# Performance work log

Hardware: AMD Instinct MI355X
Metric: run time of the kernel (lower is better)

Reference implementation:

```python
import jax, jax.numpy as jnp
import numpy as np

DIM = 512
NUM_HEADS = 8
HEAD_DIM = DIM // NUM_HEADS
MAX_SEQ_LEN = 4096
B, L = 2, 4096
LN_EPS = 1e-5


def _rope_cache(max_len, head_dim):
    inv_freq = 1.0 / (10000.0 ** (jnp.arange(0, head_dim, 2, dtype=jnp.float32) / head_dim))
    t = jnp.arange(max_len, dtype=jnp.float32)
    freqs = jnp.einsum('i,j->ij', t, inv_freq)          # [max_len, head_dim//2]
    emb = jnp.concatenate([freqs, freqs], axis=-1)       # [max_len, head_dim]
    return jnp.cos(emb)[None, None], jnp.sin(emb)[None, None]  # [1,1,max_len,head_dim]


def setup_inputs() -> dict:
    key = jax.random.key(0)
    ks = jax.random.split(key, 8)
    s_qkv = 1.0 / np.sqrt(DIM)
    x = jax.random.normal(ks[0], (B, L, DIM), dtype=jnp.float32)
    padding_mask = jax.random.bernoulli(ks[1], 0.1, (B, L))  # True = masked key
    Wqkv = jax.random.uniform(ks[2], (DIM, 3 * DIM), jnp.float32, -s_qkv, s_qkv)
    bqkv = jax.random.uniform(ks[3], (3 * DIM,), jnp.float32, -s_qkv, s_qkv)
    Wproj = jax.random.uniform(ks[4], (DIM, DIM), jnp.float32, -s_qkv, s_qkv)
    bproj = jax.random.uniform(ks[5], (DIM,), jnp.float32, -s_qkv, s_qkv)
    gamma = jnp.ones((DIM,), jnp.float32)
    beta = jnp.zeros((DIM,), jnp.float32)
    cos, sin = _rope_cache(MAX_SEQ_LEN, HEAD_DIM)
    return {"x": x, "padding_mask": padding_mask, "Wqkv": Wqkv, "bqkv": bqkv,
            "Wproj": Wproj, "bproj": bproj, "gamma": gamma, "beta": beta,
            "cos": cos, "sin": sin}


def _rotate_half(t):
    t1, t2 = jnp.split(t, 2, axis=-1)
    return jnp.concatenate([-t2, t1], axis=-1)


def reference(x, padding_mask, Wqkv, bqkv, Wproj, bproj, gamma, beta, cos, sin):
    b, l, d = x.shape
    residual = x
    qkv = (x @ Wqkv + bqkv).reshape(b, l, 3, NUM_HEADS, HEAD_DIM)
    qkv = jnp.transpose(qkv, (2, 0, 3, 1, 4))            # [3,B,H,L,hd]
    q, k, v = qkv[0], qkv[1], qkv[2]
    c = cos[:, :, :l, :]
    s = sin[:, :, :l, :]
    q = q * c + _rotate_half(q) * s
    k = k * c + _rotate_half(k) * s
    scores = jnp.einsum('bhqd,bhkd->bhqk', q, k) / jnp.sqrt(jnp.float32(HEAD_DIM))
    scores = jnp.where(padding_mask[:, None, None, :], -jnp.inf, scores)
    attn = jax.nn.softmax(scores, axis=-1)
    out = jnp.einsum('bhqk,bhkd->bhqd', attn, v)
    out = jnp.transpose(out, (0, 2, 1, 3)).reshape(b, l, d)
    y = out @ Wproj + bproj + residual
    mu = jnp.mean(y, axis=-1, keepdims=True)
    var = jnp.mean(jnp.square(y - mu), axis=-1, keepdims=True)
    return (y - mu) * jax.lax.rsqrt(var + LN_EPS) * gamma + beta
```

## Files before the change

### kernel.cpp

```cpp
#include <hip/hip_runtime.h>
#include <hip/hip_bf16.h>

typedef __bf16 bf16;
typedef __attribute__((ext_vector_type(8))) __bf16 bf16x8;
typedef __attribute__((ext_vector_type(2))) __bf16 bf16x2;
typedef __attribute__((ext_vector_type(4))) float f32x4;
typedef __attribute__((ext_vector_type(16))) float f32x16;
typedef __attribute__((ext_vector_type(4))) unsigned int u32x4;

#define DIMV 512
#define NH 8
#define HDIM 64
#define SEQ 4096
#define BB_ 2
#define M_TOT (BB_ * SEQ)
#define NQKV 1536
#define KVBLK 64

static __device__ __forceinline__ f32x4 mfma16(bf16x8 a, bf16x8 b, f32x4 c) {
  return __builtin_amdgcn_mfma_f32_16x16x32_bf16(a, b, c, 0, 0, 0);
}
static __device__ __forceinline__ f32x16 mfma32(bf16x8 a, bf16x8 b, f32x16 c) {
  return __builtin_amdgcn_mfma_f32_32x32x16_bf16(a, b, c, 0, 0, 0);
}
static __device__ __forceinline__ unsigned pk2(float a, float b) {
  bf16x2 t; t[0] = (bf16)a; t[1] = (bf16)b;
  return __builtin_bit_cast(unsigned, t);
}
static __device__ __forceinline__ void swap32(unsigned& a, unsigned& b) {
  asm("v_permlane32_swap_b32 %0, %1" : "+v"(a), "+v"(b));
}
static __device__ __forceinline__ int swz(int row, int byteoff) {
  return byteoff ^ ((row & 7) << 4);
}

__global__ void prep_w(const float* __restrict__ Wqkv, const float* __restrict__ Wproj,
                       const float* __restrict__ x, const int* __restrict__ mask,
                       bf16* __restrict__ WqkvT, bf16* __restrict__ WprojT,
                       bf16* __restrict__ xb, float* __restrict__ BBias) {
  const int t1 = DIMV * NQKV;
  const int t2 = t1 + DIMV * DIMV;
  const int t3 = t2 + M_TOT * DIMV;
  const int t4 = t3 + BB_ * SEQ;
  for (int i = blockIdx.x * blockDim.x + threadIdx.x; i < t4;
       i += gridDim.x * blockDim.x) {
    if (i < t1) {
      int n = i / DIMV, k = i - n * DIMV;
      WqkvT[i] = (bf16)Wqkv[(size_t)k * NQKV + n];
    } else if (i < t2) {
      int o = i - t1;
      int n = o / DIMV, k = o - n * DIMV;
      WprojT[o] = (bf16)Wproj[(size_t)k * DIMV + n];
    } else if (i < t3) {
      int o = i - t2;
      xb[o] = (bf16)x[o];
    } else {
      int o = i - t3;
      BBias[o] = mask[o] ? -1.0e30f : 0.0f;
    }
  }
}

__global__ __launch_bounds__(256) void gemm1_qkv_rope(
    const bf16* __restrict__ xb, const bf16* __restrict__ WT,
    const float* __restrict__ bqkv, const float* __restrict__ cosT,
    const float* __restrict__ sinT, bf16* __restrict__ Q,
    bf16* __restrict__ Kd, bf16* __restrict__ VT) {
  const int tid = threadIdx.x;
  const int wave = tid >> 6, lane = tid & 63;
  const int l16 = lane & 15, lg = lane >> 4;
  const int Mbase = blockIdx.x * 128 + (wave >> 1) * 64;
  const int Nbase = blockIdx.y * 128 + (wave & 1) * 64;
  const int gblk = (blockIdx.y * 128) >> 9;

  f32x4 acc[4][4] = {};
  if (gblk != 2) {
    for (int k0 = 0; k0 < DIMV; k0 += 32) {
      const int kb = k0 + lg * 8;
      bf16x8 af[4], bfr[4];
#pragma unroll
      for (int r = 0; r < 4; ++r) {
        af[r] = *reinterpret_cast<const bf16x8*>(
            xb + (size_t)(Mbase + r * 16 + l16) * DIMV + kb);
        bfr[r] = *reinterpret_cast<const bf16x8*>(
            WT + (size_t)(Nbase + r * 16 + l16) * DIMV + kb);
      }
#pragma unroll
      for (int mr = 0; mr < 4; ++mr)
#pragma unroll
        for (int nr = 0; nr < 4; ++nr)
          acc[mr][nr] = mfma16(af[mr], bfr[nr], acc[mr][nr]);
    }
#pragma unroll
    for (int mr = 0; mr < 4; ++mr) {
#pragma unroll
      for (int nr = 0; nr < 4; ++nr) {
#pragma unroll
        for (int j = 0; j < 4; ++j) {
          const int n = Nbase + nr * 16 + l16;
          const int m = Mbase + mr * 16 + lg * 4 + j;
          const int rem = n & 511, h = rem >> 6, d = rem & 63;
          const int b = m >> 12, l = m & 4095;
          float val = acc[mr][nr][j] + bqkv[n];
          float pairval = acc[mr][nr ^ 2][j] + bqkv[n ^ 32];
          float c = cosT[l * HDIM + d], s = sinT[l * HDIM + d];
          float o = (d < 32) ? (val * c - pairval * s) : (val * c + pairval * s);
          bf16* dst = (gblk == 0) ? Q : Kd;
          dst[((size_t)(b * NH + h) * SEQ + l) * HDIM + d] = (bf16)o;
        }
      }
    }
  } else {
    for (int k0 = 0; k0 < DIMV; k0 += 32) {
      const int kb = k0 + lg * 8;
      bf16x8 af[4], bfr[4];
#pragma unroll
      for (int r = 0; r < 4; ++r) {
        af[r] = *reinterpret_cast<const bf16x8*>(
            xb + (size_t)(Mbase + r * 16 + l16) * DIMV + kb);
        bfr[r] = *reinterpret_cast<const bf16x8*>(
            WT + (size_t)(Nbase + r * 16 + l16) * DIMV + kb);
      }
#pragma unroll
      for (int mr = 0; mr < 4; ++mr)
#pragma unroll
        for (int nr = 0; nr < 4; ++nr)
          acc[mr][nr] = mfma16(bfr[nr], af[mr], acc[mr][nr]);
    }
#pragma unroll
    for (int mr = 0; mr < 4; ++mr) {
#pragma unroll
      for (int nr = 0; nr < 4; ++nr) {
#pragma unroll
        for (int j = 0; j < 4; ++j) {
          const int n = Nbase + nr * 16 + lg * 4 + j;
          const int m = Mbase + mr * 16 + l16;
          const int rem = n & 511, h = rem >> 6, d = rem & 63;
          const int b = m >> 12, l = m & 4095;
          float val = acc[mr][nr][j] + bqkv[n];
          VT[((size_t)(b * NH + h) * HDIM + d) * SEQ + l] = (bf16)val;
        }
      }
    }
  }
}

__global__ __launch_bounds__(256) void attn_kernel(
    const bf16* __restrict__ Q, const bf16* __restrict__ Kd,
    const bf16* __restrict__ VT, const float* __restrict__ BBias,
    bf16* __restrict__ AO) {
  __shared__ __align__(16) char kv_lds[2][2][KVBLK * 128];
  __shared__ __align__(16) float lsum_lds[4][32];

  const int tid = threadIdx.x;
  const int wv = tid >> 6, lane = tid & 63;
  const int l32 = lane & 31, hi = lane >> 5;
  const int bh = blockIdx.y, b = bh >> 3, h = bh & 7;
  const int qb = blockIdx.x * 128 + wv * 32;
  const float C1 = 0.125f * 1.44269504f;

  const bf16* qrow = Q + ((size_t)bh * SEQ + qb + l32) * HDIM + 8 * hi;
  bf16x8 qfrag[4];
#pragma unroll
  for (int w = 0; w < 4; ++w)
    qfrag[w] = *reinterpret_cast<const bf16x8*>(qrow + 16 * w);

  const bf16* Kbase = Kd + (size_t)bh * SEQ * HDIM;
  const bf16* Vbase = VT + (size_t)bh * HDIM * SEQ;
  const int c0 = tid, c1 = tid + 256;
  const int kr0 = c0 >> 3, ks0 = c0 & 7;
  const int kr1 = c1 >> 3, ks1 = c1 & 7;

  const float* bbp = BBias + b * SEQ + 4 * hi;

  f32x16 o0 = {}, o1 = {};
  f32x4 lacc = {};

  bf16x8 kreg0, kreg1, vreg0, vreg1;
  {
    kreg0 = *reinterpret_cast<const bf16x8*>(Kbase + (size_t)kr0 * HDIM + ks0 * 8);
    kreg1 = *reinterpret_cast<const bf16x8*>(Kbase + (size_t)kr1 * HDIM + ks1 * 8);
    vreg0 = *reinterpret_cast<const bf16x8*>(Vbase + (size_t)kr0 * SEQ + ks0 * 8);
    vreg1 = *reinterpret_cast<const bf16x8*>(Vbase + (size_t)kr1 * SEQ + ks1 * 8);
    char* kb_ = kv_lds[0][0]; char* vb_ = kv_lds[0][1];
    *reinterpret_cast<bf16x8*>(kb_ + kr0 * 128 + swz(kr0, ks0 * 16)) = kreg0;
    *reinterpret_cast<bf16x8*>(kb_ + kr1 * 128 + swz(kr1, ks1 * 16)) = kreg1;
    *reinterpret_cast<bf16x8*>(vb_ + kr0 * 128 + swz(kr0, ks0 * 16)) = vreg0;
    *reinterpret_cast<bf16x8*>(vb_ + kr1 * 128 + swz(kr1, ks1 * 16)) = vreg1;
  }
  __syncthreads();

  const int NT = SEQ / KVBLK;
  for (int t = 0; t < NT; ++t) {
    const int cur = t & 1;
    const int kb = t * KVBLK;
    if (t + 1 < NT) {
      const int nkb = kb + KVBLK;
      kreg0 = *reinterpret_cast<const bf16x8*>(Kbase + (size_t)(nkb + kr0) * HDIM + ks0 * 8);
      kreg1 = *reinterpret_cast<const bf16x8*>(Kbase + (size_t)(nkb + kr1) * HDIM + ks1 * 8);
      vreg0 = *reinterpret_cast<const bf16x8*>(Vbase + (size_t)kr0 * SEQ + nkb + ks0 * 8);
      vreg1 = *reinterpret_cast<const bf16x8*>(Vbase + (size_t)kr1 * SEQ + nkb + ks1 * 8);
    }

    const char* kt = kv_lds[cur][0];
    const char* vt = kv_lds[cur][1];
#pragma unroll
    for (int g = 0; g < 2; ++g) {
      f32x16 S = {};
#pragma unroll
      for (int w = 0; w < 4; ++w) {
        const int row = 32 * g + l32;
        bf16x8 kf = *reinterpret_cast<const bf16x8*>(
            kt + row * 128 + swz(row, 32 * w + 16 * hi));
        S = mfma32(kf, qfrag[w], S);
      }
      float e[16];
#pragma unroll
      for (int g4 = 0; g4 < 4; ++g4) {
        f32x4 bb = *reinterpret_cast<const f32x4*>(bbp + kb + 32 * g + 8 * g4);
#pragma unroll
        for (int j = 0; j < 4; ++j) {
          float ev = __builtin_amdgcn_exp2f(fmaf(S[g4 * 4 + j], C1, bb[j]));
          e[g4 * 4 + j] = ev;
          lacc[j] += ev;
        }
      }
      unsigned p0 = pk2(e[0], e[1]),  p1 = pk2(e[2], e[3]);
      unsigned p2 = pk2(e[4], e[5]),  p3 = pk2(e[6], e[7]);
      unsigned p4 = pk2(e[8], e[9]),  p5 = pk2(e[10], e[11]);
      unsigned p6 = pk2(e[12], e[13]), p7 = pk2(e[14], e[15]);
      swap32(p0, p2); swap32(p1, p3);
      swap32(p4, p6); swap32(p5, p7);
      u32x4 u0 = {p0, p1, p2, p3}, u1 = {p4, p5, p6, p7};
      bf16x8 pa0 = __builtin_bit_cast(bf16x8, u0);
      bf16x8 pa1 = __builtin_bit_cast(bf16x8, u1);
      const int r0 = l32, r1 = 32 + l32;
      bf16x8 v00 = *reinterpret_cast<const bf16x8*>(vt + r0 * 128 + swz(r0, 64 * g + 16 * hi));
      bf16x8 v01 = *reinterpret_cast<const bf16x8*>(vt + r0 * 128 + swz(r0, 64 * g + 16 * hi + 32));
      bf16x8 v10 = *reinterpret_cast<const bf16x8*>(vt + r1 * 128 + swz(r1, 64 * g + 16 * hi));
      bf16x8 v11 = *reinterpret_cast<const bf16x8*>(vt + r1 * 128 + swz(r1, 64 * g + 16 * hi + 32));
      o0 = mfma32(pa0, v00, o0);
      o0 = mfma32(pa1, v01, o0);
      o1 = mfma32(pa0, v10, o1);
      o1 = mfma32(pa1, v11, o1);
    }

    __syncthreads();
    if (t + 1 < NT) {
      char* kb_ = kv_lds[cur ^ 1][0]; char* vb_ = kv_lds[cur ^ 1][1];
      *reinterpret_cast<bf16x8*>(kb_ + kr0 * 128 + swz(kr0, ks0 * 16)) = kreg0;
      *reinterpret_cast<bf16x8*>(kb_ + kr1 * 128 + swz(kr1, ks1 * 16)) = kreg1;
      *reinterpret_cast<bf16x8*>(vb_ + kr0 * 128 + swz(kr0, ks0 * 16)) = vreg0;
      *reinterpret_cast<bf16x8*>(vb_ + kr1 * 128 + swz(kr1, ks1 * 16)) = vreg1;
      __syncthreads();
    }
  }

  float ls = lacc[0] + lacc[1] + lacc[2] + lacc[3];
  ls += __shfl_xor(ls, 32, 64);
  if (hi == 0) lsum_lds[wv][l32] = ls;
  __syncthreads();
  f32x4 linv[4];
#pragma unroll
  for (int g = 0; g < 4; ++g) {
    f32x4 t = *reinterpret_cast<const f32x4*>(&lsum_lds[wv][8 * g + 4 * hi]);
#pragma unroll
    for (int j = 0; j < 4; ++j) linv[g][j] = 1.0f / t[j];
  }
  bf16* aop = AO + ((size_t)b * SEQ + qb) * DIMV + h * HDIM + l32;
#pragma unroll
  for (int r = 0; r < 16; ++r) {
    const int q = (r & 3) + 8 * (r >> 2) + 4 * hi;
    const float inv = linv[r >> 2][r & 3];
    aop[(size_t)q * DIMV]      = (bf16)(o0[r] * inv);
    aop[(size_t)q * DIMV + 32] = (bf16)(o1[r] * inv);
  }
}

__global__ __launch_bounds__(256) void gemm2_proj(
    const bf16* __restrict__ AO, const bf16* __restrict__ WT,
    const float* __restrict__ bproj, const float* __restrict__ x,
    float* __restrict__ Y) {
  const int tid = threadIdx.x;
  const int wave = tid >> 6, lane = tid & 63;
  const int l16 = lane & 15, lg = lane >> 4;
  const int Mbase = blockIdx.x * 128 + (wave >> 1) * 64;
  const int Nbase = blockIdx.y * 128 + (wave & 1) * 64;

  f32x4 acc[4][4] = {};
  for (int k0 = 0; k0 < DIMV; k0 += 32) {
    const int kb = k0 + lg * 8;
    bf16x8 af[4], bfr[4];
#pragma unroll
    for (int r = 0; r < 4; ++r) {
      af[r] = *reinterpret_cast<const bf16x8*>(
          AO + (size_t)(Mbase + r * 16 + l16) * DIMV + kb);
      bfr[r] = *reinterpret_cast<const bf16x8*>(
          WT + (size_t)(Nbase + r * 16 + l16) * DIMV + kb);
    }
#pragma unroll
    for (int mr = 0; mr < 4; ++mr)
#pragma unroll
      for (int nr = 0; nr < 4; ++nr)
        acc[mr][nr] = mfma16(af[mr], bfr[nr], acc[mr][nr]);
  }
#pragma unroll
  for (int mr = 0; mr < 4; ++mr)
#pragma unroll
    for (int nr = 0; nr < 4; ++nr)
#pragma unroll
      for (int j = 0; j < 4; ++j) {
        const int n = Nbase + nr * 16 + l16;
        const int m = Mbase + mr * 16 + lg * 4 + j;
        Y[(size_t)m * DIMV + n] = acc[mr][nr][j] + bproj[n] + x[(size_t)m * DIMV + n];
      }
}

__global__ __launch_bounds__(128) void ln_kernel(float* __restrict__ Y,
                                                 const float* __restrict__ gamma,
                                                 const float* __restrict__ beta) {
  const int row = blockIdx.x, tid = threadIdx.x;
  float* rp = Y + (size_t)row * DIMV;
  f32x4 v = *reinterpret_cast<const f32x4*>(rp + tid * 4);
  float s = v[0] + v[1] + v[2] + v[3];
  float q = v[0] * v[0] + v[1] * v[1] + v[2] * v[2] + v[3] * v[3];
#pragma unroll
  for (int off = 1; off < 64; off <<= 1) {
    s += __shfl_xor(s, off, 64);
    q += __shfl_xor(q, off, 64);
  }
  __shared__ float sh[4];
  if ((tid & 63) == 0) { sh[(tid >> 6) * 2] = s; sh[(tid >> 6) * 2 + 1] = q; }
  __syncthreads();
  const float ts = sh[0] + sh[2], tq = sh[1] + sh[3];
  const float mu = ts * (1.0f / DIMV);
  const float var = tq * (1.0f / DIMV) - mu * mu;
  const float rs = rsqrtf(var + 1e-5f);
  f32x4 ov;
#pragma unroll
  for (int i = 0; i < 4; ++i) {
    const int c = tid * 4 + i;
    ov[i] = (v[i] - mu) * rs * gamma[c] + beta[c];
  }
  *reinterpret_cast<f32x4*>(rp + tid * 4) = ov;
}

extern "C" void kernel_launch(void* const* d_in, const int* in_sizes, int n_in,
                              void* d_out, int out_size, void* d_ws, size_t ws_size,
                              hipStream_t stream) {
  const float* x      = (const float*)d_in[0];
  const int*   pmask  = (const int*)d_in[1];
  const float* Wqkv   = (const float*)d_in[2];
  const float* bqkv   = (const float*)d_in[3];
  const float* Wproj  = (const float*)d_in[4];
  const float* bproj  = (const float*)d_in[5];
  const float* gamma  = (const float*)d_in[6];
  const float* beta   = (const float*)d_in[7];
  const float* cosT   = (const float*)d_in[8];
  const float* sinT   = (const float*)d_in[9];
  float* out = (float*)d_out;

  char* ws = (char*)d_ws;
  const size_t MB = 1048576;
  bf16* WqkvT  = (bf16*)(ws);
  bf16* WprojT = (bf16*)(ws + 3 * MB / 2);
  bf16* Q      = (bf16*)(ws + 2 * MB);
  bf16* Kd     = (bf16*)(ws + 10 * MB);
  bf16* VT     = (bf16*)(ws + 18 * MB);
  bf16* AO     = (bf16*)(ws + 26 * MB);
  bf16* xb     = AO;
  float* BBias = (float*)(ws + 34 * MB);

  prep_w<<<2048, 256, 0, stream>>>(Wqkv, Wproj, x, pmask, WqkvT, WprojT, xb, BBias);
  gemm1_qkv_rope<<<dim3(M_TOT / 128, NQKV / 128), 256, 0, stream>>>(
      xb, WqkvT, bqkv, cosT, sinT, Q, Kd, VT);
  attn_kernel<<<dim3(SEQ / 128, BB_ * NH), 256, 0, stream>>>(Q, Kd, VT, BBias, AO);
  gemm2_proj<<<dim3(M_TOT / 128, DIMV / 128), 256, 0, stream>>>(AO, WprojT, bproj, x, out);
  ln_kernel<<<M_TOT, 128, 0, stream>>>(out, gamma, beta);
}
```

Baseline: 269.7 us.

## Stage QKV GEMM tiles in LDS via direct global-to-LDS loads; drop attention barrier

```diff
diff --git a/kernel.cpp b/kernel.cpp
--- a/kernel.cpp
+++ b/kernel.cpp
@@ -32,6 +32,11 @@
 }
 static __device__ __forceinline__ int swz(int row, int byteoff) {
   return byteoff ^ ((row & 7) << 4);
+}
+static __device__ __forceinline__ void gload_lds16(const bf16* g, bf16* lds) {
+  __builtin_amdgcn_global_load_lds(
+      (const __attribute__((address_space(1))) unsigned int*)g,
+      (__attribute__((address_space(3))) unsigned int*)lds, 16, 0, 0);
 }
 
 __global__ void prep_w(const float* __restrict__ Wqkv, const float* __restrict__ Wproj,
@@ -66,31 +71,54 @@
     const float* __restrict__ bqkv, const float* __restrict__ cosT,
     const float* __restrict__ sinT, bf16* __restrict__ Q,
     bf16* __restrict__ Kd, bf16* __restrict__ VT) {
+  __shared__ __align__(16) bf16 As[128 * 32];
+  __shared__ __align__(16) bf16 Bs[128 * 32];
   const int tid = threadIdx.x;
   const int wave = tid >> 6, lane = tid & 63;
   const int l16 = lane & 15, lg = lane >> 4;
-  const int Mbase = blockIdx.x * 128 + (wave >> 1) * 64;
-  const int Nbase = blockIdx.y * 128 + (wave & 1) * 64;
+  const int Mblk = blockIdx.x * 128, Nblk = blockIdx.y * 128;
+  const int Mbase = Mblk + (wave >> 1) * 64;
+  const int Nbase = Nblk + (wave & 1) * 64;
   const int gblk = (blockIdx.y * 128) >> 9;
 
+  const bf16* Ag = xb + (size_t)(Mblk + wave * 32 + (lane >> 2)) * DIMV + (lane & 3) * 8;
+  const bf16* Bg = WT + (size_t)(Nblk + wave * 32 + (lane >> 2)) * DIMV + (lane & 3) * 8;
+  bf16* AsW = As + wave * 32 * 32;
+  bf16* BsW = Bs + wave * 32 * 32;
+
   f32x4 acc[4][4] = {};
-  if (gblk != 2) {
-    for (int k0 = 0; k0 < DIMV; k0 += 32) {
-      const int kb = k0 + lg * 8;
-      bf16x8 af[4], bfr[4];
-#pragma unroll
-      for (int r = 0; r < 4; ++r) {
-        af[r] = *reinterpret_cast<const bf16x8*>(
-            xb + (size_t)(Mbase + r * 16 + l16) * DIMV + kb);
-        bfr[r] = *reinterpret_cast<const bf16x8*>(
-            WT + (size_t)(Nbase + r * 16 + l16) * DIMV + kb);
-      }
+  for (int k0 = 0; k0 < DIMV; k0 += 32) {
+    gload_lds16(Ag + k0, AsW);
+    gload_lds16(Ag + k0 + (size_t)16 * DIMV, AsW + 16 * 32);
+    gload_lds16(Bg + k0, BsW);
+    gload_lds16(Bg + k0 + (size_t)16 * DIMV, BsW + 16 * 32);
+    __syncthreads();
+
+    bf16x8 af[4], bfr[4];
+#pragma unroll
+    for (int r = 0; r < 4; ++r) {
+      af[r] = *reinterpret_cast<const bf16x8*>(
+          As + ((wave >> 1) * 64 + r * 16 + l16) * 32 + lg * 8);
+      bfr[r] = *reinterpret_cast<const bf16x8*>(
+          Bs + ((wave & 1) * 64 + r * 16 + l16) * 32 + lg * 8);
+    }
+    if (gblk != 2) {
 #pragma unroll
       for (int mr = 0; mr < 4; ++mr)
 #pragma unroll
         for (int nr = 0; nr < 4; ++nr)
           acc[mr][nr] = mfma16(af[mr], bfr[nr], acc[mr][nr]);
-    }
+    } else {
+#pragma unroll
+      for (int mr = 0; mr < 4; ++mr)
+#pragma unroll
+        for (int nr = 0; nr < 4; ++nr)
+          acc[mr][nr] = mfma16(bfr[nr], af[mr], acc[mr][nr]);
+    }
+    __syncthreads();
+  }
+
+  if (gblk != 2) {
 #pragma unroll
     for (int mr = 0; mr < 4; ++mr) {
 #pragma unroll
@@ -111,22 +139,6 @@
       }
     }
   } else {
-    for (int k0 = 0; k0 < DIMV; k0 += 32) {
-      const int kb = k0 + lg * 8;
-      bf16x8 af[4], bfr[4];
-#pragma unroll
-      for (int r = 0; r < 4; ++r) {
-        af[r] = *reinterpret_cast<const bf16x8*>(
-            xb + (size_t)(Mbase + r * 16 + l16) * DIMV + kb);
-        bfr[r] = *reinterpret_cast<const bf16x8*>(
-            WT + (size_t)(Nbase + r * 16 + l16) * DIMV + kb);
-      }
-#pragma unroll
-      for (int mr = 0; mr < 4; ++mr)
-#pragma unroll
-        for (int nr = 0; nr < 4; ++nr)
-          acc[mr][nr] = mfma16(bfr[nr], af[mr], acc[mr][nr]);
-    }
 #pragma unroll
     for (int mr = 0; mr < 4; ++mr) {
 #pragma unroll
@@ -245,15 +257,14 @@
       o1 = mfma32(pa1, v11, o1);
     }
 
-    __syncthreads();
     if (t + 1 < NT) {
       char* kb_ = kv_lds[cur ^ 1][0]; char* vb_ = kv_lds[cur ^ 1][1];
       *reinterpret_cast<bf16x8*>(kb_ + kr0 * 128 + swz(kr0, ks0 * 16)) = kreg0;
       *reinterpret_cast<bf16x8*>(kb_ + kr1 * 128 + swz(kr1, ks1 * 16)) = kreg1;
       *reinterpret_cast<bf16x8*>(vb_ + kr0 * 128 + swz(kr0, ks0 * 16)) = vreg0;
       *reinterpret_cast<bf16x8*>(vb_ + kr1 * 128 + swz(kr1, ks1 * 16)) = vreg1;
-      __syncthreads();
-    }
+    }
+    __syncthreads();
   }
 
   float ls = lacc[0] + lacc[1] + lacc[2] + lacc[3];
```

Result: faster. 255.2 us (-5.4%).
